# Performance work log

Hardware: AMD Instinct MI355X
Metric: run time of the kernel (lower is better)

## Reference

```python
import jax, jax.numpy as jnp
import numpy as np
from jax import lax

N_NODES = 4096
WINDOW = 288
SLIDE = 12
ENC_STEPS = 12
DEC_STEPS = 12
HID = 64
EMB = 64
PRED = 12
C1, C2 = 32, 64
KSZ, STR = 10, 2
OUT_LEN = 66  # ((288-10)//2+1 -> 140; (140-10)//2+1 -> 66)
EPS = 1e-5


def _conv1d(x, w, b, stride):
    # x: [N, Cin, L], w: [Cout, Cin, K]
    y = lax.conv_general_dilated(x, w, (stride,), 'VALID',
                                 dimension_numbers=('NCH', 'OIH', 'NCH'))
    return y + b[None, :, None]


def _bn(x, g, b):
    # BatchNorm1d training-mode stats over (batch, length) per channel
    m = x.mean(axis=(0, 2), keepdims=True)
    v = x.var(axis=(0, 2), keepdims=True)
    return (x - m) * jax.lax.rsqrt(v + EPS) * g[None, :, None] + b[None, :, None]


def _embed(x, conv1_w, conv1_b, conv2_w, conv2_b, bn1_g, bn1_b, bn2_g, bn2_b,
           fcconv_w, fcconv_b, fc_w, fc_b):
    # x: [N, WINDOW] -> [N, EMB]
    x = x[:, None, :]                                   # [N,1,W]
    x = _bn(jax.nn.relu(_conv1d(x, conv1_w, conv1_b, STR)), bn1_g, bn1_b)
    x = _bn(jax.nn.relu(_conv1d(x, conv2_w, conv2_b, STR)), bn2_g, bn2_b)
    x = jax.nn.relu(_conv1d(x, fcconv_w, fcconv_b, 1))  # [N,1,OUT_LEN]
    x = jnp.einsum('ncl,le->nce', x, fc_w) + fc_b       # [N,1,EMB]
    # NOTE: original code calls F.relu(x) but discards the result -> no relu here
    return x[:, 0, :]


def _gconv(x, adj, W, b):
    # diffusion conv: [x, A x, 2A(Ax) - x] (K=2, includes identity term)
    x1 = adj @ x
    x2 = 2.0 * (adj @ x1) - x
    return jnp.concatenate([x, x1, x2], axis=-1) @ W + b


def _dcgru_cell(x, h, adj, Wg, bg, Wc, bc):
    ru = jax.nn.sigmoid(_gconv(jnp.concatenate([x, h], -1), adj, Wg, bg))
    r, u = jnp.split(ru, 2, axis=-1)
    c = jnp.tanh(_gconv(jnp.concatenate([x, r * h], -1), adj, Wc, bc))
    return u * h + (1.0 - u) * c


def setup_inputs() -> dict:
    key = jax.random.key(0)
    ks = jax.random.split(key, 20)
    n_mat = 3  # K+1 diffusion matrices
    gin = (EMB + HID) * n_mat
    inp = {
        'inputs': jax.random.normal(ks[0], (N_NODES, (ENC_STEPS + DEC_STEPS - 1) * SLIDE + WINDOW), jnp.float32),
        'targets': jax.random.normal(ks[1], (N_NODES, DEC_STEPS * PRED), jnp.float32),
        'conv1_w': jax.random.normal(ks[3], (C1, 1, KSZ), jnp.float32) * 0.1,
        'conv1_b': jnp.zeros((C1,), jnp.float32),
        'conv2_w': jax.random.normal(ks[4], (C2, C1, KSZ), jnp.float32) * 0.1,
        'conv2_b': jnp.zeros((C2,), jnp.float32),
        'bn1_g': jnp.ones((C1,), jnp.float32), 'bn1_b': jnp.zeros((C1,), jnp.float32),
        'bn2_g': jnp.ones((C2,), jnp.float32), 'bn2_b': jnp.zeros((C2,), jnp.float32),
        'fcconv_w': jax.random.normal(ks[5], (1, C2, 1), jnp.float32) * 0.1,
        'fcconv_b': jnp.zeros((1,), jnp.float32),
        'fc_w': jax.random.normal(ks[6], (OUT_LEN, EMB), jnp.float32) * (1.0 / np.sqrt(OUT_LEN)),
        'fc_b': jnp.zeros((EMB,), jnp.float32),
        'enc_Wg': jax.random.normal(ks[7], (gin, 2 * HID), jnp.float32) * (1.0 / np.sqrt(gin)),
        'enc_bg': jnp.ones((2 * HID,), jnp.float32),
        'enc_Wc': jax.random.normal(ks[8], (gin, HID), jnp.float32) * (1.0 / np.sqrt(gin)),
        'enc_bc': jnp.zeros((HID,), jnp.float32),
        'dec_Wg': jax.random.normal(ks[9], (gin, 2 * HID), jnp.float32) * (1.0 / np.sqrt(gin)),
        'dec_bg': jnp.ones((2 * HID,), jnp.float32),
        'dec_Wc': jax.random.normal(ks[10], (gin, HID), jnp.float32) * (1.0 / np.sqrt(gin)),
        'dec_bc': jnp.zeros((HID,), jnp.float32),
        'pred_w': jax.random.normal(ks[11], (HID, PRED), jnp.float32) * (1.0 / np.sqrt(HID)),
        'pred_b': jnp.full((PRED,), 0.1, jnp.float32),
    }
    a = jax.random.uniform(ks[2], (N_NODES, N_NODES), jnp.float32)
    inp['adj'] = a / a.sum(axis=-1, keepdims=True)  # row-stochastic adjacency
    return inp


def reference(inputs, targets, adj,
              conv1_w, conv1_b, conv2_w, conv2_b, bn1_g, bn1_b, bn2_g, bn2_b,
              fcconv_w, fcconv_b, fc_w, fc_b,
              enc_Wg, enc_bg, enc_Wc, enc_bc,
              dec_Wg, dec_bg, dec_Wc, dec_bc,
              pred_w, pred_b):
    n = inputs.shape[0]
    # windowed views: idx[i] = i*SLIDE, 24 windows of length WINDOW
    idx = SLIDE * jnp.arange(ENC_STEPS + DEC_STEPS)
    wins = inputs[:, idx[:, None] + jnp.arange(WINDOW)]        # [N, 24, W]
    wins = jnp.transpose(wins, (1, 0, 2))                      # [24, N, W]
    embs = jax.vmap(lambda w: _embed(w, conv1_w, conv1_b, conv2_w, conv2_b,
                                     bn1_g, bn1_b, bn2_g, bn2_b,
                                     fcconv_w, fcconv_b, fc_w, fc_b))(wins)  # [24,N,EMB]
    enc_x, dec_x = embs[:ENC_STEPS], embs[ENC_STEPS:]

    h0 = jnp.zeros((n, HID), inputs.dtype)
    def enc_step(h, x):
        return _dcgru_cell(x, h, adj, enc_Wg, enc_bg, enc_Wc, enc_bc), None
    h_enc, _ = lax.scan(enc_step, h0, enc_x)

    # decoder: each step uses the SAME encoder hidden state (as in original code)
    dec_h = jax.vmap(lambda x: _dcgru_cell(x, h_enc, adj, dec_Wg, dec_bg, dec_Wc, dec_bc))(dec_x)  # [12,N,HID]
    preds = dec_h @ pred_w + pred_b                             # [12,N,PRED]
    return jnp.transpose(preds, (1, 0, 2)).reshape(n, DEC_STEPS * PRED)
```

## Files before the change

### kernel.cpp

```cpp
#include <hip/hip_runtime.h>
#include <hip/hip_bf16.h>
#include <math.h>

#define NN     4096
#define INLEN  564
#define NT     24
#define NC1    32
#define NC2    64
#define KS     10
#define EPS    1e-5f

typedef short s8v __attribute__((ext_vector_type(8)));
typedef short s4v __attribute__((ext_vector_type(4)));
typedef float f4v __attribute__((ext_vector_type(4)));
typedef float f2v __attribute__((ext_vector_type(2)));

static const long O_COLS   = 0;
static const long O_COLSQ  = 8960;
static const long O_STATS  = 17920;
static const long O_H      = 20992;
static const long ZERO_FLOATS = 291328;
static const long O_A1     = 291328;
static const long O_D1     = 292096;
static const long O_CB2    = 292864;
static const long O_W2B    = 532480;
static const long O_G1P    = 778240;
static const long O_Y2     = 19128320;
static const long O_EMBS   = 28041216;
static const long O_ADJB   = 532480;
static const long O_PP     = 8921088;
static const long O_X      = 13115392;
static const long O_T1     = 13901824;
static const long O_T1T    = 14426112;
static const long O_T2     = 14688256;
static const long O_RH     = 15212544;
static const long O_RHT    = 15474688;
static const long O_P1S    = 15605760;
static const long O_P1ST   = 15867904;
static const long O_P2S    = 15998976;
static const long O_UE     = 16261120;
static const long O_X12    = 16392192;
static const long O_XT12   = 22683648;
static const long O_EB     = 16392192;
static const long O_EBT    = 20062208;
static const long O_AE1    = 21897216;
static const long O_AE1T   = 25567232;
static const long O_AE2    = 27795456;
static const long O_RHB    = 31465472;
static const long O_P1B    = 34611200;
static const long O_P1BT   = O_PP;
static const long O_P2B    = O_X;
static const long O_HD     = O_PP;

struct Src { const float* p; int ld; int off; int tmul; };

static __device__ __forceinline__ float cvt_bf(short s) {
  return __uint_as_float(((unsigned)(unsigned short)s) << 16);
}
static __device__ __forceinline__ short bf16bits(float v) {
  __hip_bfloat16_raw r = __hip_bfloat16_raw(__float2bfloat16(v));
  return (short)r.x;
}

__global__ __launch_bounds__(256) void k_conv1n(const float* __restrict__ inp,
    const float* __restrict__ w1, const float* __restrict__ b1,
    __hip_bfloat16* __restrict__ g1p) {
  __shared__ float xin[INLEN];
  __shared__ float wl[320];
  __shared__ float bl[32];
  int n = blockIdx.x, tid = threadIdx.x;
  for (int i=tid; i<INLEN; i+=256) xin[i] = inp[(long)n*INLEN + i];
  for (int i=tid; i<320; i+=256) wl[i] = w1[i];
  if (tid < 32)  bl[tid] = b1[tid];
  __syncthreads();
  int c = tid & 31, pb = tid >> 5;
  float wreg[KS];
  #pragma unroll
  for (int k=0;k<KS;k++) wreg[k] = wl[c*KS+k];
  float bias = bl[c];
  for (int p = pb; p < 280; p += 8) {
    float acc = 0.f;
    if (p < 278) {
      acc = bias;
      #pragma unroll
      for (int k=0;k<KS;k++) acc = fmaf(wreg[k], xin[2*p+k], acc);
      acc = fmaxf(acc, 0.f);
    }
    g1p[((long)n*280 + p)*32 + c] = __float2bfloat16(acc);
  }
}

__global__ __launch_bounds__(256) void k_colsum2(const __hip_bfloat16* __restrict__ g1p,
    float* __restrict__ colS, float* __restrict__ colSQ) {
  int gid = blockIdx.x*256 + threadIdx.x;
  int cg = gid % 1120, chunk = gid / 1120;
  int col0 = cg*8;
  float s[8], sq[8];
  #pragma unroll
  for (int j=0;j<8;j++) { s[j]=0.f; sq[j]=0.f; }
  int n0 = chunk*128;
  const short* gp = (const short*)g1p;
  for (int n=n0; n<n0+128; n++) {
    s8v v = *(const s8v*)(gp + (long)n*8960 + col0);
    #pragma unroll
    for (int j=0;j<8;j++) { float f = cvt_bf(v[j]); s[j]+=f; sq[j]+=f*f; }
  }
  #pragma unroll
  for (int j=0;j<8;j++) { atomicAdd(&colS[col0+j], s[j]); atomicAdd(&colSQ[col0+j], sq[j]); }
}

__global__ __launch_bounds__(64) void k_bn1aff(const float* __restrict__ colS,
    const float* __restrict__ colSQ, const float* __restrict__ g, const float* __restrict__ b,
    float* __restrict__ a1, float* __restrict__ d1) {
  int i = blockIdx.x*64 + threadIdx.x;
  if (i >= NT*NC1) return;
  int t = i / NC1, c = i % NC1;
  float s=0.f, sq=0.f;
  for (int p=6*t; p<6*t+140; p++) { s += colS[p*32+c]; sq += colSQ[p*32+c]; }
  float cnt = 4096.f*140.f;
  float m = s/cnt;
  float v = sq/cnt - m*m;
  float a = g[c]*rsqrtf(v+EPS);
  a1[i] = a;
  d1[i] = b[c] - m*a;
}

__global__ __launch_bounds__(256) void k_w2b(const float* __restrict__ w2,
    const float* __restrict__ b2, const float* __restrict__ a1, const float* __restrict__ d1,
    __hip_bfloat16* __restrict__ w2b, float* __restrict__ cb2) {
  int i = blockIdx.x*256 + threadIdx.x;
  if (i >= NT*NC2) return;
  int t = i>>6, c2 = i&63;
  float cb = b2[c2];
  for (int c1=0;c1<NC1;c1++) {
    float a = a1[t*32+c1], d = d1[t*32+c1];
    float wsum = 0.f;
    for (int k=0;k<KS;k++) {
      float wv = w2[(c2*32+c1)*KS+k];
      wsum += wv;
      w2b[(((long)t*10 + k)*64 + c2)*32 + c1] = __float2bfloat16(wv*a);
    }
    cb += wsum*d;
  }
  cb2[i] = cb;
}

__global__ __launch_bounds__(256) void k_conv2m(const __hip_bfloat16* __restrict__ g1p,
    const __hip_bfloat16* __restrict__ w2b, const float* __restrict__ cb2,
    __hip_bfloat16* __restrict__ y2, float* __restrict__ stats, int t) {
  __shared__ __attribute__((aligned(16))) short patch[4*140*40];
  __shared__ float sS[64], sQ[64];
  int tid = threadIdx.x, w = tid>>6, lane = tid&63;
  int n0 = blockIdx.x*4;
  if (tid < 64) { sS[tid]=0.f; sQ[tid]=0.f; }
  const short* gp = (const short*)g1p;
  for (int f = tid; f < 2240; f += 256) {
    int nn = f / 560, rr = f % 560;
    int row = rr >> 2, kq = rr & 3;
    s8v v = *(const s8v*)(gp + ((long)(n0+nn)*280 + 6*t + row)*32 + kq*8);
    *(s8v*)&patch[(nn*140 + row)*40 + kq*8] = v;
  }
  __syncthreads();
  int q = lane>>4, m = lane&15;
  f4v acc[5][4];
  #pragma unroll
  for (int a=0;a<5;a++)
    #pragma unroll
    for (int b=0;b<4;b++) acc[a][b] = (f4v){0.f,0.f,0.f,0.f};
  const short* wb = (const short*)w2b + (long)t*10*64*32;
  for (int s=0; s<10; s++) {
    int j = s>>1, r = s&1;
    s8v bfr[4];
    #pragma unroll
    for (int ng=0; ng<4; ng++)
      bfr[ng] = *(const s8v*)(wb + (long)(s*64 + ng*16 + m)*32 + q*8);
    #pragma unroll
    for (int mg=0; mg<5; mg++) {
      int l2 = mg*16 + m;
      int u = l2 + j; u = (u>69)?69:u;
      s8v afr = *(const s8v*)&patch[(w*140 + 2*u + r)*40 + q*8];
      #pragma unroll
      for (int ng=0; ng<4; ng++)
        acc[mg][ng] = __builtin_amdgcn_mfma_f32_16x16x32_bf16(afr, bfr[ng], acc[mg][ng], 0,0,0);
    }
  }
  int node = n0 + w;
  float s1a[4]={0,0,0,0}, s2a[4]={0,0,0,0};
  #pragma unroll
  for (int mg=0; mg<5; mg++) {
    int l2b = mg*16 + q*4;
    #pragma unroll
    for (int ng=0; ng<4; ng++) {
      int c2 = ng*16 + m;
      float cbv = cb2[t*64 + c2];
      float vv[4];
      #pragma unroll
      for (int rr=0; rr<4; rr++) {
        float v = fmaxf(acc[mg][ng][rr] + cbv, 0.f);
        vv[rr] = v;
        if (l2b + rr < 66) { s1a[ng] += v; s2a[ng] += v*v; }
      }
      long base = ((long)node*64 + c2)*68 + l2b;
      if (mg < 4) {
        s4v o;
        #pragma unroll
        for (int rr=0; rr<4; rr++) o[rr] = bf16bits(vv[rr]);
        *(s4v*)((short*)y2 + base) = o;
      } else {
        for (int rr=0; rr<4; rr++) if (l2b+rr < 66) y2[base+rr] = __float2bfloat16(vv[rr]);
      }
    }
  }
  #pragma unroll
  for (int ng=0; ng<4; ng++) {
    atomicAdd(&sS[ng*16+m], s1a[ng]);
    atomicAdd(&sQ[ng*16+m], s2a[ng]);
  }
  __syncthreads();
  if (tid < 64) {
    atomicAdd(&stats[t*128+tid], sS[tid]);
    atomicAdd(&stats[t*128+64+tid], sQ[tid]);
  }
}

__global__ __launch_bounds__(256) void k_pass2(const __hip_bfloat16* __restrict__ y2,
    const float* __restrict__ stats, const float* __restrict__ bn2g, const float* __restrict__ bn2b,
    const float* __restrict__ fcvw, const float* __restrict__ fcvb,
    const float* __restrict__ fcW, const float* __restrict__ fcB,
    float* __restrict__ embs, int t) {
  __shared__ __attribute__((aligned(16))) short yb[4*64*68];
  __shared__ float fw[66*64];
  __shared__ float fwa[64], cfcs[64];
  __shared__ float zbuf[4][68];
  int tid = threadIdx.x;
  int n0 = blockIdx.x*4;
  const short* yg = (const short*)y2;
  for (int f=tid; f<2176; f+=256)
    *(s8v*)&yb[f*8] = *(const s8v*)(yg + (long)n0*64*68 + f*8);
  for (int i=tid; i<66*64; i+=256) fw[i] = fcW[i];
  if (tid < 64) {
    float cnt = 4096.f*66.f;
    float m = stats[t*128+tid]/cnt;
    float v = stats[t*128+64+tid]/cnt - m*m;
    float a = bn2g[tid]*rsqrtf(v+EPS);
    float d = bn2b[tid] - m*a;
    fwa[tid]  = fcvw[tid]*a;
    cfcs[tid] = fcvw[tid]*d;
  }
  __syncthreads();
  float cfc = fcvb[0];
  #pragma unroll 8
  for (int c=0;c<64;c++) cfc += cfcs[c];
  for (int idx=tid; idx<4*66; idx+=256) {
    int nn = idx/66, l = idx%66;
    float z = cfc;
    #pragma unroll 8
    for (int c=0;c<64;c++) z = fmaf(fwa[c], cvt_bf(yb[(nn*64+c)*68 + l]), z);
    zbuf[nn][l] = fmaxf(z, 0.f);
  }
  __syncthreads();
  int nn = tid>>6, e = tid&63;
  float acc = fcB[e];
  for (int l=0;l<66;l++) acc = fmaf(zbuf[nn][l], fw[l*64+e], acc);
  embs[((long)t*NN + n0+nn)*64 + e] = acc;
}

__global__ __launch_bounds__(256) void k_cvtadj(const float* __restrict__ adj,
    __hip_bfloat16* __restrict__ adjb) {
  long gid = ((long)blockIdx.x*256 + threadIdx.x)*4;
  float4 v = *(const float4*)(adj + gid);
  adjb[gid+0] = __float2bfloat16(v.x);
  adjb[gid+1] = __float2bfloat16(v.y);
  adjb[gid+2] = __float2bfloat16(v.z);
  adjb[gid+3] = __float2bfloat16(v.w);
}

template<int BN>
__global__ __launch_bounds__(256) void k_mmb(const __hip_bfloat16* __restrict__ A,
    const __hip_bfloat16* __restrict__ Bt, float* __restrict__ P,
    int N, int kchunk, long zoff,
    float* __restrict__ dst, const float* __restrict__ ref,
    __hip_bfloat16* __restrict__ dstT, int mode, int writeT, int zsplit) {
  constexpr int BM = 64;
  constexpr int WN = BN/2;
  constexpr int MI = 2;
  constexpr int NJ = WN/16;
  constexpr int AIT = 2;
  constexpr int BIT = BN*8/256;
  __shared__ __attribute__((aligned(16))) short As[BM*64];
  __shared__ __attribute__((aligned(16))) short Bs[BN*64];
  int tid = threadIdx.x;
  int w = tid >> 6, lane = tid & 63;
  int wm = w >> 1, wn = w & 1;
  int q = lane >> 4, m = lane & 15;
  long Mb = (long)blockIdx.x * BM;
  int Nb = blockIdx.y * BN;
  int k0 = blockIdx.z * kchunk;
  const short* Ag = (const short*)A;
  const short* Bg = (const short*)Bt;
  s8v arA[AIT], brA[BIT], arB[AIT], brB[BIT];

  auto loadAr = [&](s8v* d, int kb){
    #pragma unroll
    for (int i2=0;i2<AIT;i2++){ int f=tid+i2*256; int kq=f&7, row=f>>3;
      d[i2] = *(const s8v*)(Ag + (Mb+row)*4096 + kb + kq*8); } };
  auto loadBr = [&](s8v* d, int kb){
    #pragma unroll
    for (int i2=0;i2<BIT;i2++){ int f=tid+i2*256; int kq=f&7, col=f>>3;
      d[i2] = *(const s8v*)(Bg + (long)(Nb+col)*4096 + kb + kq*8); } };

  f4v acc[MI][NJ];
  #pragma unroll
  for (int i=0;i<MI;i++)
    #pragma unroll
    for (int j=0;j<NJ;j++) acc[i][j] = (f4v){0.f,0.f,0.f,0.f};

  auto writeS = [&](s8v* a, s8v* b){
    #pragma unroll
    for (int i2=0;i2<AIT;i2++){ int f=tid+i2*256; int kq=f&7, row=f>>3;
      *(s8v*)&As[(row*8 + (kq ^ (row&7)))*8] = a[i2]; }
    #pragma unroll
    for (int i2=0;i2<BIT;i2++){ int f=tid+i2*256; int kq=f&7, col=f>>3;
      *(s8v*)&Bs[(col*8 + (kq ^ (col&7)))*8] = b[i2]; } };
  auto compute = [&](){
    #pragma unroll
    for (int h2=0; h2<2; ++h2) {
      s8v af[MI], bfv[NJ];
      #pragma unroll
      for (int i=0;i<MI;i++) {
        int row = wm*32 + i*16 + m;
        af[i] = *(const s8v*)&As[(row*8 + ((h2*4+q) ^ (row&7)))*8];
      }
      #pragma unroll
      for (int j=0;j<NJ;j++) {
        int col = wn*WN + j*16 + m;
        bfv[j] = *(const s8v*)&Bs[(col*8 + ((h2*4+q) ^ (col&7)))*8];
      }
      #pragma unroll
      for (int i=0;i<MI;i++)
        #pragma unroll
        for (int j=0;j<NJ;j++)
          acc[i][j] = __builtin_amdgcn_mfma_f32_16x16x32_bf16(af[i], bfv[j], acc[i][j], 0, 0, 0);
    } };

  loadAr(arA, k0);      loadBr(brA, k0);
  loadAr(arB, k0+64);   loadBr(brB, k0+64);
  int kiters = kchunk >> 6;
  for (int it = 0; it < kiters; it += 2) {
    __syncthreads();
    writeS(arA, brA);
    __syncthreads();
    { int kn = (it+2 < kiters) ? k0 + (it+2)*64 : k0;
      loadAr(arA, kn); loadBr(brA, kn); }
    compute();
    __syncthreads();
    writeS(arB, brB);
    __syncthreads();
    { int kn = (it+3 < kiters) ? k0 + (it+3)*64 : k0;
      loadAr(arB, kn); loadBr(brB, kn); }
    compute();
  }

  if (zsplit > 1) {
    float* pp = P + (long)blockIdx.z * zoff;
    #pragma unroll
    for (int i=0;i<MI;i++) {
      long row0 = Mb + wm*32 + i*16 + q*4;
      #pragma unroll
      for (int j=0;j<NJ;j++) {
        int col = Nb + wn*WN + j*16 + m;
        #pragma unroll
        for (int r=0;r<4;r++) pp[(row0+r)*N + col] = acc[i][j][r];
      }
    }
  } else {
    #pragma unroll
    for (int i=0;i<MI;i++) {
      long row0 = Mb + wm*32 + i*16 + q*4;
      #pragma unroll
      for (int j=0;j<NJ;j++) {
        int col = Nb + wn*WN + j*16 + m;
        float vr[4];
        #pragma unroll
        for (int r=0;r<4;r++) {
          long idx = (row0+r)*N + col;
          float v = acc[i][j][r];
          if (mode) v = 2.f*v - ref[idx];
          dst[idx] = v;
          vr[r] = v;
        }
        if (writeT) {
          s4v o;
          #pragma unroll
          for (int r=0;r<4;r++) o[r] = bf16bits(vr[r]);
          *(s4v*)((short*)dstT + (long)col*4096 + row0) = o;
        }
      }
    }
  }
}

__global__ __launch_bounds__(256) void k_redT(const float* __restrict__ P,
    float* __restrict__ dst, const float* __restrict__ ref,
    __hip_bfloat16* __restrict__ dstT, int ldc, int ksplit, long zoff, int mode,
    int writeF, int writeT) {
  __shared__ float tile[64][65];
  int tid = threadIdx.x;
  int n0 = blockIdx.x*64, c0 = blockIdx.y*64;
  for (int i=0; i<16; i++) {
    int flat = i*256 + tid;
    int cc = flat & 63, nn = flat >> 6;
    long idx = (long)(n0+nn)*ldc + c0+cc;
    float v = P[idx];
    for (int s=1; s<ksplit; s++) v += P[(long)s*zoff + idx];
    if (mode) v = 2.f*v - ref[idx];
    if (writeF) dst[idx] = v;
    tile[nn][cc] = v;
  }
  __syncthreads();
  if (writeT) {
    for (int i=0; i<16; i++) {
      int flat = i*256 + tid;
      int nn = flat & 63, cc = flat >> 6;
      dstT[(long)(c0+cc)*4096 + n0+nn] = __float2bfloat16(tile[nn][cc]);
    }
  }
}

__global__ __launch_bounds__(256) void k_prepX(const float* __restrict__ embs,
    float* __restrict__ X12, __hip_bfloat16* __restrict__ Xt12) {
  __shared__ float tile[64][65];
  int tid = threadIdx.x;
  int n0 = blockIdx.x*64, c0 = blockIdx.y*64, t = blockIdx.z;
  float* X = X12 + (long)t*524288;
  __hip_bfloat16* Xt = Xt12 + (long)t*524288;
  for (int i=0; i<16; i++) {
    int flat = i*256 + tid;
    int cc = flat & 63, nn = flat >> 6;
    int col = c0 + cc, n = n0 + nn;
    float v = (col < 64) ? embs[((long)t*NN + n)*64 + col] : 0.f;
    X[(long)n*128 + col] = v;
    tile[nn][cc] = v;
  }
  __syncthreads();
  for (int i=0; i<16; i++) {
    int flat = i*256 + tid;
    int nn = flat & 63, cc = flat >> 6;
    Xt[(long)(c0+cc)*4096 + n0+nn] = __float2bfloat16(tile[nn][cc]);
  }
}

__global__ __launch_bounds__(256) void k_gatherE(const float* __restrict__ embs,
    const float* __restrict__ h, float* __restrict__ Eb, __hip_bfloat16* __restrict__ Ebt) {
  __shared__ float tile[64][65];
  int tid = threadIdx.x;
  int n0 = blockIdx.x*64, c0 = blockIdx.y*64;
  for (int i=0; i<16; i++) {
    int flat = i*256 + tid;
    int cc = flat & 63, nn = flat >> 6;
    int col = c0 + cc, n = n0 + nn;
    float v;
    if (col < 768)      v = embs[((long)(12 + (col>>6))*NN + n)*64 + (col & 63)];
    else if (col < 832) v = h[(long)n*64 + (col - 768)];
    else                v = 0.f;
    Eb[(long)n*896 + col] = v;
    tile[nn][cc] = v;
  }
  __syncthreads();
  for (int i=0; i<16; i++) {
    int flat = i*256 + tid;
    int nn = flat & 63, cc = flat >> 6;
    Ebt[(long)(c0+cc)*4096 + n0+nn] = __float2bfloat16(tile[nn][cc]);
  }
}

template<int RPT>
__global__ __launch_bounds__(256) void k_ggemm2(
    Src s0, Src s1, Src s2, Src s3, Src s4, Src s5,
    const float* __restrict__ W, const float* __restrict__ bias, int N, int mode,
    float* __restrict__ o1, int ld1, int t1, __hip_bfloat16* __restrict__ o1t,
    __hip_bfloat16* __restrict__ o2, const float* __restrict__ h,
    float* __restrict__ xnext, __hip_bfloat16* __restrict__ xtnext) {
  constexpr int BM = 16*RPT;
  __shared__ float Ags[32][BM+4];
  __shared__ float Bgs[32][68];
  int tid = threadIdx.x;
  long Mb = (long)blockIdx.x * BM;
  int Nb = blockIdx.y * 64;
  int tr = tid >> 4, tc = tid & 15;
  float acc[RPT][4];
  #pragma unroll
  for (int a=0;a<RPT;a++)
    #pragma unroll
    for (int b=0;b<4;b++) acc[a][b] = 0.f;
  float ar[2*RPT], br[8];
  auto pick = [&](int c)->Src {
    switch (c >> 1) {
      case 0: return s0; case 1: return s1; case 2: return s2;
      case 3: return s3; case 4: return s4; default: return s5;
    } };
  auto loadA = [&](int c){
    Src S = pick(c); int cc0 = (c & 1)*32;
    #pragma unroll
    for (int h0=0; h0<2*RPT; h0++) {
      int idx = tid + h0*256;
      int kk = idx & 31, mm = idx >> 5;
      long row = Mb + mm; int tt = (int)(row >> 12); int n = (int)(row & 4095);
      ar[h0] = S.p[(long)n*S.ld + S.off + S.tmul*(tt*64) + cc0 + kk];
    } };
  auto loadB = [&](int c){
    #pragma unroll
    for (int h0=0; h0<8; h0++) {
      int idx = tid + h0*256;
      int kk = idx >> 6, cc = idx & 63;
      br[h0] = W[(long)(c*32+kk)*N + Nb + cc];
    } };
  loadA(0); loadB(0);
  for (int c=0; c<12; c++) {
    __syncthreads();
    #pragma unroll
    for (int h0=0; h0<2*RPT; h0++) {
      int idx = tid + h0*256;
      int kk = idx & 31, mm = idx >> 5;
      Ags[kk][mm] = ar[h0];
    }
    #pragma unroll
    for (int h0=0; h0<8; h0++)     { int idx = tid + h0*256; Bgs[idx >> 6][idx & 63] = br[h0]; }
    __syncthreads();
    if (c < 11) { loadA(c+1); loadB(c+1); }
    #pragma unroll
    for (int kk=0; kk<32; kk++) {
      f4v b4 = *(const f4v*)&Bgs[kk][tc*4];
      if constexpr (RPT == 2) {
        f2v a0 = *(const f2v*)&Ags[kk][tr*2];
        #pragma unroll
        for (int rr=0; rr<2; rr++)
          #pragma unroll
          for (int j=0; j<4; j++)
            acc[rr][j] = fmaf(a0[rr], b4[j], acc[rr][j]);
      } else {
        float a0 = Ags[kk][tr];
        #pragma unroll
        for (int j=0; j<4; j++)
          acc[0][j] = fmaf(a0, b4[j], acc[0][j]);
      }
    }
  }
  #pragma unroll
  for (int rr=0; rr<RPT; rr++) {
    long row = Mb + tr*RPT + rr;
    int tt = (int)(row >> 12); int n = (int)(row & 4095);
    #pragma unroll
    for (int j=0; j<4; j++) {
      int col = Nb + tc*4 + j;
      float g = acc[rr][j] + bias[col];
      if (mode == 0) {
        float sg = 1.f/(1.f + expf(-g));
        if (col < 64) {
          float v = sg * h[(long)n*64 + col];
          o1[(long)n*ld1 + (long)t1*tt*64 + col] = v;
          o1t[((long)t1*tt*64 + col)*4096 + n] = __float2bfloat16(v);
        } else {
          o2[(long)row*64 + (col - 64)] = __float2bfloat16(sg);
        }
      } else {
        float uu = __bfloat162float(o2[(long)row*64 + col]);
        float v = uu*h[(long)n*64 + col] + (1.f - uu)*tanhf(g);
        o1[(long)row*64 + col] = v;
        if (xnext) {
          xnext[(long)n*128 + 64 + col] = v;
          xtnext[(long)(64 + col)*4096 + n] = __float2bfloat16(v);
        }
      }
    }
  }
}

__global__ __launch_bounds__(256) void k_ggemm3(
    Src s0, Src s1, Src s2, Src s3, Src s4, Src s5,
    const float* __restrict__ W, const float* __restrict__ bias, int N, int mode,
    float* __restrict__ o1, int ld1, int t1, __hip_bfloat16* __restrict__ o1t,
    __hip_bfloat16* __restrict__ o2, const float* __restrict__ h) {
  __shared__ __attribute__((aligned(16))) short As[64*32];
  __shared__ __attribute__((aligned(16))) short Bs[64*32];
  int tid = threadIdx.x;
  int w = tid >> 6, lane = tid & 63;
  int wm = w >> 1, wn = w & 1;
  int q = lane >> 4, m = lane & 15;
  long Mb = (long)blockIdx.x * 64;
  int Nb = blockIdx.y * 64;
  int arow = tid >> 2, ag = tid & 3;
  int bnn  = tid & 63, bg = tid >> 6;
  auto pick = [&](int c)->Src {
    switch (c >> 1) {
      case 0: return s0; case 1: return s1; case 2: return s2;
      case 3: return s3; case 4: return s4; default: return s5;
    } };
  f4v a0r, a1r; float wr[8];
  auto loadA = [&](int c){
    Src S = pick(c); int cc0 = (c & 1)*32;
    long row = Mb + arow; int tt = (int)(row >> 12); int n = (int)(row & 4095);
    const float* p = S.p + (long)n*S.ld + S.off + S.tmul*(tt*64) + cc0 + ag*8;
    a0r = *(const f4v*)p; a1r = *(const f4v*)(p+4);
  };
  auto loadB = [&](int c){
    #pragma unroll
    for (int jj=0;jj<8;jj++) wr[jj] = W[(long)(c*32 + bg*8 + jj)*N + Nb + bnn];
  };
  f4v acc[2][2];
  #pragma unroll
  for (int i=0;i<2;i++)
    #pragma unroll
    for (int j=0;j<2;j++) acc[i][j] = (f4v){0.f,0.f,0.f,0.f};
  loadA(0); loadB(0);
  for (int c=0; c<12; c++) {
    __syncthreads();
    {
      s8v va;
      #pragma unroll
      for (int jj=0;jj<4;jj++) { va[jj] = bf16bits(a0r[jj]); va[4+jj] = bf16bits(a1r[jj]); }
      *(s8v*)&As[(arow*4 + (ag ^ (arow&3)))*8] = va;
      s8v vb;
      #pragma unroll
      for (int jj=0;jj<8;jj++) vb[jj] = bf16bits(wr[jj]);
      *(s8v*)&Bs[(bnn*4 + (bg ^ (bnn&3)))*8] = vb;
    }
    __syncthreads();
    if (c < 11) { loadA(c+1); loadB(c+1); }
    s8v af[2], bfv[2];
    #pragma unroll
    for (int i=0;i<2;i++) {
      int row = wm*32 + i*16 + m;
      af[i] = *(const s8v*)&As[(row*4 + (q ^ (row&3)))*8];
    }
    #pragma unroll
    for (int j=0;j<2;j++) {
      int col = wn*32 + j*16 + m;
      bfv[j] = *(const s8v*)&Bs[(col*4 + (q ^ (col&3)))*8];
    }
    #pragma unroll
    for (int i=0;i<2;i++)
      #pragma unroll
      for (int j=0;j<2;j++)
        acc[i][j] = __builtin_amdgcn_mfma_f32_16x16x32_bf16(af[i], bfv[j], acc[i][j], 0, 0, 0);
  }
  #pragma unroll
  for (int i=0;i<2;i++) {
    #pragma unroll
    for (int r=0;r<4;r++) {
      long row = Mb + wm*32 + i*16 + q*4 + r;
      int tt = (int)(row >> 12); int n = (int)(row & 4095);
      #pragma unroll
      for (int j=0;j<2;j++) {
        int col = Nb + wn*32 + j*16 + m;
        float g = acc[i][j][r] + bias[col];
        if (mode == 0) {
          float sg = 1.f/(1.f + expf(-g));
          if (col < 64) {
            float v = sg * h[(long)n*64 + col];
            o1[(long)n*ld1 + (long)t1*tt*64 + col] = v;
            o1t[((long)t1*tt*64 + col)*4096 + n] = __float2bfloat16(v);
          } else {
            o2[(long)row*64 + (col - 64)] = __float2bfloat16(sg);
          }
        } else {
          float uu = __bfloat162float(o2[(long)row*64 + col]);
          o1[(long)row*64 + col] = uu*h[(long)n*64 + col] + (1.f - uu)*tanhf(g);
        }
      }
    }
  }
}

__global__ __launch_bounds__(256) void k_pred(const float* __restrict__ hd,
    const float* __restrict__ pw, const float* __restrict__ pb, float* __restrict__ out) {
  int gid = blockIdx.x*256 + threadIdx.x;
  int wid = gid >> 6;
  int lane = threadIdx.x & 63;
  if (wid >= 12*NN) return;
  int t = wid >> 12, n = wid & 4095;
  float hv = hd[(long)wid*64 + lane];
  float res = 0.f;
  #pragma unroll
  for (int p=0;p<12;p++) {
    float v = hv * pw[lane*12 + p];
    #pragma unroll
    for (int off=32; off>0; off>>=1) v += __shfl_xor(v, off, 64);
    if (lane == p) res = v + pb[p];
  }
  if (lane < 12) out[(long)n*144 + t*12 + lane] = res;
}

extern "C" void kernel_launch(void* const* d_in, const int* in_sizes, int n_in,
                              void* d_out, int out_size, void* d_ws, size_t ws_size,
                              hipStream_t stream) {
  const float* inp  = (const float*)d_in[0];
  const float* c1w  = (const float*)d_in[2];
  const float* c1b  = (const float*)d_in[3];
  const float* c2w  = (const float*)d_in[4];
  const float* c2b  = (const float*)d_in[5];
  const float* bn1g = (const float*)d_in[6];
  const float* bn1b = (const float*)d_in[7];
  const float* bn2g = (const float*)d_in[8];
  const float* bn2b = (const float*)d_in[9];
  const float* fcvw = (const float*)d_in[10];
  const float* fcvb = (const float*)d_in[11];
  const float* fcW  = (const float*)d_in[12];
  const float* fcB  = (const float*)d_in[13];
  const float* eWg  = (const float*)d_in[14];
  const float* ebg  = (const float*)d_in[15];
  const float* eWc  = (const float*)d_in[16];
  const float* ebc  = (const float*)d_in[17];
  const float* dWg  = (const float*)d_in[18];
  const float* dbg  = (const float*)d_in[19];
  const float* dWc  = (const float*)d_in[20];
  const float* dbc  = (const float*)d_in[21];
  const float* pw   = (const float*)d_in[22];
  const float* pb   = (const float*)d_in[23];
  const float* adj  = (const float*)d_in[n_in-1];
  for (int i=0;i<n_in;i++) if (in_sizes[i] == NN*NN) adj = (const float*)d_in[i];

  float* ws = (float*)d_ws;
  float* colS  = ws + O_COLS;
  float* colSQ = ws + O_COLSQ;
  float* stats = ws + O_STATS;
  float* h     = ws + O_H;
  float* a1    = ws + O_A1;
  float* d1    = ws + O_D1;
  float* cb2   = ws + O_CB2;
  __hip_bfloat16* w2b = (__hip_bfloat16*)(ws + O_W2B);
  __hip_bfloat16* g1p = (__hip_bfloat16*)(ws + O_G1P);
  __hip_bfloat16* y2  = (__hip_bfloat16*)(ws + O_Y2);
  float* embs  = ws + O_EMBS;
  __hip_bfloat16* adjb = (__hip_bfloat16*)(ws + O_ADJB);
  float* Pp    = ws + O_PP;
  float* T1    = ws + O_T1;
  __hip_bfloat16* T1t = (__hip_bfloat16*)(ws + O_T1T);
  float* T2    = ws + O_T2;
  float* rh    = ws + O_RH;
  __hip_bfloat16* rht = (__hip_bfloat16*)(ws + O_RHT);
  float* P1s   = ws + O_P1S;
  __hip_bfloat16* P1st = (__hip_bfloat16*)(ws + O_P1ST);
  float* P2s   = ws + O_P2S;
  __hip_bfloat16* ue  = (__hip_bfloat16*)(ws + O_UE);
  float* X12   = ws + O_X12;
  __hip_bfloat16* Xt12 = (__hip_bfloat16*)(ws + O_XT12);
  float* Eb    = ws + O_EB;
  __hip_bfloat16* Ebt = (__hip_bfloat16*)(ws + O_EBT);
  float* AE1   = ws + O_AE1;
  __hip_bfloat16* AE1t = (__hip_bfloat16*)(ws + O_AE1T);
  float* AE2   = ws + O_AE2;
  float* RHb   = ws + O_RHB;
  float* P1B   = ws + O_P1B;
  float* P2B   = ws + O_P2B;
  float* hd    = ws + O_HD;
  __hip_bfloat16* RHbt = Ebt;
  __hip_bfloat16* P1Bt = (__hip_bfloat16*)(ws + O_P1BT);
  __hip_bfloat16* ud   = AE1t;

  auto S = [](const float* p, int ld, int off, int tmul){ Src s; s.p=p; s.ld=ld; s.off=off; s.tmul=tmul; return s; };

  hipMemsetAsync(ws, 0, ZERO_FLOATS*sizeof(float), stream);

  k_conv1n<<<4096, 256, 0, stream>>>(inp, c1w, c1b, g1p);
  k_colsum2<<<140, 256, 0, stream>>>(g1p, colS, colSQ);
  k_bn1aff<<<12, 64, 0, stream>>>(colS, colSQ, bn1g, bn1b, a1, d1);
  k_w2b   <<<6, 256, 0, stream>>>(c2w, c2b, a1, d1, w2b, cb2);
  for (int t=0; t<NT; t++) {
    k_conv2m<<<1024, 256, 0, stream>>>(g1p, w2b, cb2, y2, stats, t);
    k_pass2 <<<1024, 256, 0, stream>>>(y2, stats, bn2g, bn2b, fcvw, fcvb, fcW, fcB, embs, t);
  }

  k_cvtadj<<<16384, 256, 0, stream>>>(adj, adjb);

  k_prepX<<<dim3(64,2,12), 256, 0, stream>>>(embs, X12, Xt12);
  for (int t=0; t<12; t++) {
    const float* et = embs + (long)t*NN*64;
    float* X_t = X12 + (long)t*524288;
    __hip_bfloat16* Xt_t = Xt12 + (long)t*524288;
    float* Xn  = (t < 11) ? X12 + (long)(t+1)*524288 : (float*)nullptr;
    __hip_bfloat16* Xtn = (t < 11) ? Xt12 + (long)(t+1)*524288 : (__hip_bfloat16*)nullptr;
    k_mmb<128><<<dim3(64,1,8), 256, 0, stream>>>(adjb, Xt_t, Pp, 128, 512, 4096L*128,
        (float*)nullptr, (const float*)nullptr, (__hip_bfloat16*)nullptr, 0, 0, 8);
    k_redT<<<dim3(64,2), 256, 0, stream>>>(Pp, T1, (const float*)nullptr, T1t,
        128, 8, 4096L*128, 0, 1, 1);
    k_mmb<128><<<dim3(64,1,8), 256, 0, stream>>>(adjb, T1t, Pp, 128, 512, 4096L*128,
        (float*)nullptr, (const float*)nullptr, (__hip_bfloat16*)nullptr, 0, 0, 8);
    k_redT<<<dim3(64,2), 256, 0, stream>>>(Pp, T2, X_t, (__hip_bfloat16*)nullptr,
        128, 8, 4096L*128, 1, 1, 0);
    k_ggemm2<2><<<dim3(128,2), 256, 0, stream>>>(
        S(X_t,128,0,0), S(X_t,128,64,0), S(T1,128,0,0), S(T1,128,64,0), S(T2,128,0,0), S(T2,128,64,0),
        eWg, ebg, 128, 0, rh, 64, 0, rht, ue, h, (float*)nullptr, (__hip_bfloat16*)nullptr);
    k_mmb<64><<<dim3(64,1,8), 256, 0, stream>>>(adjb, rht, Pp, 64, 512, 4096L*64,
        (float*)nullptr, (const float*)nullptr, (__hip_bfloat16*)nullptr, 0, 0, 8);
    k_redT<<<dim3(64,1), 256, 0, stream>>>(Pp, P1s, (const float*)nullptr, P1st,
        64, 8, 4096L*64, 0, 1, 1);
    k_mmb<64><<<dim3(64,1,8), 256, 0, stream>>>(adjb, P1st, Pp, 64, 512, 4096L*64,
        (float*)nullptr, (const float*)nullptr, (__hip_bfloat16*)nullptr, 0, 0, 8);
    k_redT<<<dim3(64,1), 256, 0, stream>>>(Pp, P2s, rh, (__hip_bfloat16*)nullptr,
        64, 8, 4096L*64, 1, 1, 0);
    k_ggemm2<1><<<dim3(256,1), 256, 0, stream>>>(
        S(et,64,0,0), S(rh,64,0,0), S(T1,128,0,0), S(P1s,64,0,0), S(T2,128,0,0), S(P2s,64,0,0),
        eWc, ebc, 64, 1, h, 0, 0, (__hip_bfloat16*)nullptr, ue, h, Xn, Xtn);
  }

  k_gatherE<<<dim3(64,14), 256, 0, stream>>>(embs, h, Eb, Ebt);
  k_mmb<128><<<dim3(64,7,1), 256, 0, stream>>>(adjb, Ebt, Pp, 896, 4096, 0,
      AE1, (const float*)nullptr, AE1t, 0, 1, 1);
  k_mmb<128><<<dim3(64,7,1), 256, 0, stream>>>(adjb, AE1t, Pp, 896, 4096, 0,
      AE2, Eb, (__hip_bfloat16*)nullptr, 1, 0, 1);
  k_ggemm3<<<dim3(768,2), 256, 0, stream>>>(
      S(Eb,896,0,1), S(Eb,896,768,0), S(AE1,896,0,1), S(AE1,896,768,0), S(AE2,896,0,1), S(AE2,896,768,0),
      dWg, dbg, 128, 0, RHb, 768, 1, RHbt, ud, h);
  k_mmb<128><<<dim3(64,6,1), 256, 0, stream>>>(adjb, RHbt, Pp, 768, 4096, 0,
      P1B, (const float*)nullptr, P1Bt, 0, 1, 1);
  k_mmb<128><<<dim3(64,6,1), 256, 0, stream>>>(adjb, P1Bt, Pp, 768, 4096, 0,
      P2B, RHb, (__hip_bfloat16*)nullptr, 1, 0, 1);
  k_ggemm3<<<dim3(768,1), 256, 0, stream>>>(
      S(Eb,896,0,1), S(RHb,768,0,1), S(AE1,896,0,1), S(P1B,768,0,1), S(AE2,896,0,1), S(P2B,768,0,1),
      dWc, dbc, 64, 1, hd, 0, 0, (__hip_bfloat16*)nullptr, ud, h);

  k_pred<<<12288, 256, 0, stream>>>(hd, pw, pb, (float*)d_out);
}
```

Before: 4.922 ms.

## Recompute conv2 in second pass instead of storing intermediate activations

```diff
diff --git a/kernel.cpp b/kernel.cpp
--- a/kernel.cpp
+++ b/kernel.cpp
@@ -25,7 +25,6 @@
 static const long O_CB2    = 292864;
 static const long O_W2B    = 532480;
 static const long O_G1P    = 778240;
-static const long O_Y2     = 19128320;
 static const long O_EMBS   = 28041216;
 static const long O_ADJB   = 532480;
 static const long O_PP     = 8921088;
@@ -145,9 +144,9 @@
   cb2[i] = cb;
 }
 
-__global__ __launch_bounds__(256) void k_conv2m(const __hip_bfloat16* __restrict__ g1p,
+__global__ __launch_bounds__(256) void k_conv2s(const __hip_bfloat16* __restrict__ g1p,
     const __hip_bfloat16* __restrict__ w2b, const float* __restrict__ cb2,
-    __hip_bfloat16* __restrict__ y2, float* __restrict__ stats, int t) {
+    float* __restrict__ stats, int t) {
   __shared__ __attribute__((aligned(16))) short patch[4*140*40];
   __shared__ float sS[64], sQ[64];
   int tid = threadIdx.x, w = tid>>6, lane = tid&63;
@@ -184,30 +183,17 @@
         acc[mg][ng] = __builtin_amdgcn_mfma_f32_16x16x32_bf16(afr, bfr[ng], acc[mg][ng], 0,0,0);
     }
   }
-  int node = n0 + w;
   float s1a[4]={0,0,0,0}, s2a[4]={0,0,0,0};
   #pragma unroll
   for (int mg=0; mg<5; mg++) {
     int l2b = mg*16 + q*4;
     #pragma unroll
     for (int ng=0; ng<4; ng++) {
-      int c2 = ng*16 + m;
-      float cbv = cb2[t*64 + c2];
-      float vv[4];
+      float cbv = cb2[t*64 + ng*16 + m];
       #pragma unroll
       for (int rr=0; rr<4; rr++) {
         float v = fmaxf(acc[mg][ng][rr] + cbv, 0.f);
-        vv[rr] = v;
         if (l2b + rr < 66) { s1a[ng] += v; s2a[ng] += v*v; }
-      }
-      long base = ((long)node*64 + c2)*68 + l2b;
-      if (mg < 4) {
-        s4v o;
-        #pragma unroll
-        for (int rr=0; rr<4; rr++) o[rr] = bf16bits(vv[rr]);
-        *(s4v*)((short*)y2 + base) = o;
-      } else {
-        for (int rr=0; rr<4; rr++) if (l2b+rr < 66) y2[base+rr] = __float2bfloat16(vv[rr]);
       }
     }
   }
@@ -223,46 +209,93 @@
   }
 }
 
-__global__ __launch_bounds__(256) void k_pass2(const __hip_bfloat16* __restrict__ y2,
-    const float* __restrict__ stats, const float* __restrict__ bn2g, const float* __restrict__ bn2b,
-    const float* __restrict__ fcvw, const float* __restrict__ fcvb,
-    const float* __restrict__ fcW, const float* __restrict__ fcB,
-    float* __restrict__ embs, int t) {
-  __shared__ __attribute__((aligned(16))) short yb[4*64*68];
+__global__ __launch_bounds__(256) void k_conv2f(const __hip_bfloat16* __restrict__ g1p,
+    const __hip_bfloat16* __restrict__ w2b, const float* __restrict__ cb2,
+    const float* __restrict__ stats, const float* __restrict__ bn2g,
+    const float* __restrict__ bn2b, const float* __restrict__ fcvw,
+    const float* __restrict__ fcvb, const float* __restrict__ fcW,
+    const float* __restrict__ fcB, float* __restrict__ embs, int t) {
+  __shared__ __attribute__((aligned(16))) short patch[4*140*40];
   __shared__ float fw[66*64];
   __shared__ float fwa[64], cfcs[64];
-  __shared__ float zbuf[4][68];
-  int tid = threadIdx.x;
+  __shared__ float zbuf[4][80];
+  int tid = threadIdx.x, w = tid>>6, lane = tid&63;
   int n0 = blockIdx.x*4;
-  const short* yg = (const short*)y2;
-  for (int f=tid; f<2176; f+=256)
-    *(s8v*)&yb[f*8] = *(const s8v*)(yg + (long)n0*64*68 + f*8);
+  const short* gp = (const short*)g1p;
+  for (int f = tid; f < 2240; f += 256) {
+    int nn = f / 560, rr = f % 560;
+    int row = rr >> 2, kq = rr & 3;
+    s8v v = *(const s8v*)(gp + ((long)(n0+nn)*280 + 6*t + row)*32 + kq*8);
+    *(s8v*)&patch[(nn*140 + row)*40 + kq*8] = v;
+  }
   for (int i=tid; i<66*64; i+=256) fw[i] = fcW[i];
   if (tid < 64) {
     float cnt = 4096.f*66.f;
-    float m = stats[t*128+tid]/cnt;
-    float v = stats[t*128+64+tid]/cnt - m*m;
-    float a = bn2g[tid]*rsqrtf(v+EPS);
-    float d = bn2b[tid] - m*a;
+    float mm_ = stats[t*128+tid]/cnt;
+    float vv_ = stats[t*128+64+tid]/cnt - mm_*mm_;
+    float a = bn2g[tid]*rsqrtf(vv_+EPS);
+    float d = bn2b[tid] - mm_*a;
     fwa[tid]  = fcvw[tid]*a;
     cfcs[tid] = fcvw[tid]*d;
   }
   __syncthreads();
+  int q = lane>>4, m = lane&15;
+  f4v acc[5][4];
+  #pragma unroll
+  for (int a=0;a<5;a++)
+    #pragma unroll
+    for (int b=0;b<4;b++) acc[a][b] = (f4v){0.f,0.f,0.f,0.f};
+  const short* wb = (const short*)w2b + (long)t*10*64*32;
+  for (int s=0; s<10; s++) {
+    int j = s>>1, r = s&1;
+    s8v bfr[4];
+    #pragma unroll
+    for (int ng=0; ng<4; ng++)
+      bfr[ng] = *(const s8v*)(wb + (long)(s*64 + ng*16 + m)*32 + q*8);
+    #pragma unroll
+    for (int mg=0; mg<5; mg++) {
+      int l2 = mg*16 + m;
+      int u = l2 + j; u = (u>69)?69:u;
+      s8v afr = *(const s8v*)&patch[(w*140 + 2*u + r)*40 + q*8];
+      #pragma unroll
+      for (int ng=0; ng<4; ng++)
+        acc[mg][ng] = __builtin_amdgcn_mfma_f32_16x16x32_bf16(afr, bfr[ng], acc[mg][ng], 0,0,0);
+    }
+  }
   float cfc = fcvb[0];
   #pragma unroll 8
   for (int c=0;c<64;c++) cfc += cfcs[c];
-  for (int idx=tid; idx<4*66; idx+=256) {
-    int nn = idx/66, l = idx%66;
-    float z = cfc;
-    #pragma unroll 8
-    for (int c=0;c<64;c++) z = fmaf(fwa[c], cvt_bf(yb[(nn*64+c)*68 + l]), z);
-    zbuf[nn][l] = fmaxf(z, 0.f);
+  float cbv[4], fwv[4];
+  #pragma unroll
+  for (int ng=0; ng<4; ng++) {
+    cbv[ng] = cb2[t*64 + ng*16 + m];
+    fwv[ng] = fwa[ng*16 + m];
+  }
+  #pragma unroll
+  for (int mg=0; mg<5; mg++) {
+    #pragma unroll
+    for (int rr=0; rr<4; rr++) {
+      float p = 0.f;
+      #pragma unroll
+      for (int ng=0; ng<4; ng++) {
+        float v = fmaxf(acc[mg][ng][rr] + cbv[ng], 0.f);
+        p = fmaf(fwv[ng], v, p);
+      }
+      p += __shfl_xor(p, 1, 64);
+      p += __shfl_xor(p, 2, 64);
+      p += __shfl_xor(p, 4, 64);
+      p += __shfl_xor(p, 8, 64);
+      if (m == 0) {
+        int l = mg*16 + q*4 + rr;
+        zbuf[w][l] = fmaxf(cfc + p, 0.f);
+      }
+    }
   }
   __syncthreads();
   int nn = tid>>6, e = tid&63;
-  float acc = fcB[e];
-  for (int l=0;l<66;l++) acc = fmaf(zbuf[nn][l], fw[l*64+e], acc);
-  embs[((long)t*NN + n0+nn)*64 + e] = acc;
+  float a2 = fcB[e];
+  for (int l=0;l<66;l++) a2 = fmaf(zbuf[nn][l], fw[l*64+e], a2);
+  embs[((long)t*NN + n0+nn)*64 + e] = a2;
 }
 
 __global__ __launch_bounds__(256) void k_cvtadj(const float* __restrict__ adj,
@@ -730,7 +763,6 @@
   float* cb2   = ws + O_CB2;
   __hip_bfloat16* w2b = (__hip_bfloat16*)(ws + O_W2B);
   __hip_bfloat16* g1p = (__hip_bfloat16*)(ws + O_G1P);
-  __hip_bfloat16* y2  = (__hip_bfloat16*)(ws + O_Y2);
   float* embs  = ws + O_EMBS;
   __hip_bfloat16* adjb = (__hip_bfloat16*)(ws + O_ADJB);
   float* Pp    = ws + O_PP;
@@ -767,8 +799,9 @@
   k_bn1aff<<<12, 64, 0, stream>>>(colS, colSQ, bn1g, bn1b, a1, d1);
   k_w2b   <<<6, 256, 0, stream>>>(c2w, c2b, a1, d1, w2b, cb2);
   for (int t=0; t<NT; t++) {
-    k_conv2m<<<1024, 256, 0, stream>>>(g1p, w2b, cb2, y2, stats, t);
-    k_pass2 <<<1024, 256, 0, stream>>>(y2, stats, bn2g, bn2b, fcvw, fcvb, fcW, fcB, embs, t);
+    k_conv2s<<<1024, 256, 0, stream>>>(g1p, w2b, cb2, stats, t);
+    k_conv2f<<<1024, 256, 0, stream>>>(g1p, w2b, cb2, stats, bn2g, bn2b,
+                                       fcvw, fcvb, fcW, fcB, embs, t);
   }
 
   k_cvtadj<<<16384, 256, 0, stream>>>(adj, adjb);
```

Measured after the change: 5.025 ms. 1.02x slower.
